# Kernel optimization log

Hardware: AMD Instinct MI355X
Metric: run time of the kernel (lower is better)

The kernel has to match this reference:

```python
import jax, jax.numpy as jnp
import numpy as np

N_CHANNELS = 22
N_PATCHES = 64
N_NODES = N_CHANNELS * N_PATCHES  # 1408
EMBED_DIM = 256
N_HEADS = 4
HEAD_DIM = EMBED_DIM // N_HEADS
ALPHA = 0.15
TOP_P = 0.85
DIST_THRESH = 0.55
BATCH = 16

TCP_PAIRS = [('FP1','F7'),('F7','T3'),('T3','T5'),('T5','O1'),('FP2','F8'),('F8','T4'),('T4','T6'),('T6','O2'),('FP1','F3'),('F3','C3'),('C3','P3'),('P3','O1'),('FP2','F4'),('F4','C4'),('C4','P4'),('P4','O2'),('A1','T3'),('T3','C3'),('C3','CZ'),('CZ','C4'),('C4','T4'),('T4','A2')]
_ELECTRODE_3D = {'FP1':(-0.31,0.95,0.0),'FP2':(0.31,0.95,0.0),'F7':(-0.81,0.59,0.0),'F3':(-0.55,0.67,0.5),'FZ':(0.0,0.71,0.71),'F4':(0.55,0.67,0.5),'F8':(0.81,0.59,0.0),'T3':(-1.0,0.0,0.0),'C3':(-0.57,0.0,0.82),'CZ':(0.0,0.0,1.0),'C4':(0.57,0.0,0.82),'T4':(1.0,0.0,0.0),'T5':(-0.81,-0.59,0.0),'P3':(-0.55,-0.67,0.5),'PZ':(0.0,-0.71,0.71),'P4':(0.55,-0.67,0.5),'T6':(0.81,-0.59,0.0),'O1':(-0.31,-0.95,0.0),'O2':(0.31,-0.95,0.0),'A1':(-1.05,0.0,-0.3),'A2':(1.05,0.0,-0.3)}


def _build_masks():
    # channel positions = midpoint of each bipolar TCP pair -> [22,3]
    ch_pos = np.array([(np.array(_ELECTRODE_3D[a]) + np.array(_ELECTRODE_3D[b])) / 2.0 for a, b in TCP_PAIRS])
    d = np.linalg.norm(ch_pos[:, None, :] - ch_pos[None, :, :], axis=-1)
    ch_adj = (d < DIST_THRESH).astype(np.float32)
    np.fill_diagonal(ch_adj, 0.0)
    # node = ch * n_patches + t ; spatial edges only between same t: kron(ch_adj, I_P)
    spatial = np.kron(ch_adj, np.eye(N_PATCHES, dtype=np.float32))
    # temporal: same channel, |p - p'| == 1
    T = np.zeros((N_PATCHES, N_PATCHES), dtype=np.float32)
    idx = np.arange(N_PATCHES - 1)
    T[idx, idx + 1] = 1.0
    T[idx + 1, idx] = 1.0
    temporal = np.kron(np.eye(N_CHANNELS, dtype=np.float32), T)
    return jnp.asarray(temporal), jnp.asarray(spatial)


def setup_inputs() -> dict:
    key = jax.random.key(0)
    ks = jax.random.split(key, 8)
    D, H, HD = EMBED_DIM, N_HEADS, HEAD_DIM
    s = 1.0 / np.sqrt(D)
    x = jax.random.normal(ks[0], (BATCH, N_NODES, D), dtype=jnp.float32)
    proj_w = jax.random.uniform(ks[1], (H, HD, D), jnp.float32, -s, s)
    gate_w = jax.random.uniform(ks[2], (3, D), jnp.float32, -s, s)
    gate_b = jax.random.uniform(ks[3], (3,), jnp.float32, -s, s)
    score_w1 = jax.random.uniform(ks[4], (D // 2, D), jnp.float32, -s, s)
    score_b1 = jax.random.uniform(ks[5], (D // 2,), jnp.float32, -s, s)
    s2 = 1.0 / np.sqrt(D // 2)
    score_w2 = jax.random.uniform(ks[6], (1, D // 2), jnp.float32, -s2, s2)
    score_b2 = jax.random.uniform(ks[7], (1,), jnp.float32, -s2, s2)
    threshold = jnp.asarray(0.5, dtype=jnp.float32)
    temporal_mask, spatial_mask = _build_masks()
    return {"x": x, "proj_w": proj_w, "gate_w": gate_w, "gate_b": gate_b,
            "score_w1": score_w1, "score_b1": score_b1, "score_w2": score_w2,
            "score_b2": score_b2, "threshold": threshold,
            "temporal_mask": temporal_mask, "spatial_mask": spatial_mask}


def _safe_dist(d2):
    d2 = jnp.maximum(d2, 0.0)
    return jnp.where(d2 > 0, jnp.sqrt(jnp.where(d2 > 0, d2, 1.0)), 0.0)


def reference(x, proj_w, gate_w, gate_b, score_w1, score_b1, score_w2, score_b2,
              threshold, temporal_mask, spatial_mask):
    B, N, D = x.shape
    H = proj_w.shape[0]
    k = max(1, int(N * ALPHA))
    b_idx = jnp.arange(B)[:, None, None]
    r_idx = jnp.arange(N)[None, :, None]

    # ---- MultiHeadDistanceKNN: mean over heads of (knn-mask * gaussian sim) ----
    adj = jnp.zeros((B, N, N), x.dtype)
    for h in range(H):
        z = x @ proj_w[h].T                                  # [B,N,hd]
        sq = jnp.sum(z * z, axis=-1)                         # [B,N]
        d2 = sq[:, :, None] + sq[:, None, :] - 2.0 * jnp.einsum('bnd,bmd->bnm', z, z)
        dist = _safe_dist(d2)                                # [B,N,N]
        _, topk_idx = jax.lax.top_k(-dist, k)                # k smallest dists
        m = jnp.zeros((B, N, N), x.dtype).at[b_idx, r_idx, topk_idx].set(1.0)
        m = jnp.maximum(m, jnp.swapaxes(m, -1, -2))          # symmetrize
        sim = jnp.exp(-dist * dist / (2.0 * jnp.mean(dist) ** 2 + 1e-8))
        adj = adj + sim * m
    adj = adj / H

    # ---- Temporal / Spatial filters (fixed masks) ----
    adj_t = adj * temporal_mask[None]
    adj_s = adj * spatial_mask[None]

    # ---- Pathological filter: MLP node score -> outer product -> soft gate ----
    h1 = jax.nn.gelu(x @ score_w1.T + score_b1, approximate=False)
    scores = jax.nn.sigmoid((h1 @ score_w2.T + score_b2)[..., 0])    # [B,N]
    edge_w = scores[:, :, None] * scores[:, None, :]
    adj_p = adj * jax.nn.sigmoid((edge_w - threshold) * 10.0)

    # ---- NoisyGatedRouter (eval: no noise): softmax -> top-p truncate -> renorm ----
    probs = jax.nn.softmax(x @ gate_w.T + gate_b, axis=-1)           # [B,N,3]
    order = jnp.argsort(-probs, axis=-1)
    sp = jnp.take_along_axis(probs, order, axis=-1)
    keep = (jnp.cumsum(sp, axis=-1) - sp) < TOP_P
    sp = sp * keep.astype(sp.dtype)
    inv = jnp.argsort(order, axis=-1)
    w = jnp.take_along_axis(sp, inv, axis=-1)                        # scatter back
    w = w / (jnp.sum(w, axis=-1, keepdims=True) + 1e-8)              # [B,N,3]

    # ---- Mix filters with per-edge weights (w_i + w_j)/2 ----
    out = jnp.zeros_like(adj)
    for f, a in enumerate((adj_t, adj_s, adj_p)):
        wf = w[:, :, f]
        ewf = (wf[:, :, None] + wf[:, None, :]) * 0.5
        out = out + a * ewf
    return out
```

## Files before the change

### kernel.cpp

```cpp
#include <hip/hip_runtime.h>
#include <math.h>

typedef __attribute__((ext_vector_type(8))) short bf16x8;
typedef __attribute__((ext_vector_type(4))) float f32x4;

__device__ __forceinline__ float wsum64(float v) {
#pragma unroll
  for (int d = 32; d > 0; d >>= 1) v += __shfl_xor(v, d, 64);
  return v;
}

__device__ __forceinline__ unsigned short f2bf(float f) {
  unsigned u = __float_as_uint(f);
  u = (u + 0x7FFFu + ((u >> 16) & 1u)) >> 16;
  return (unsigned short)u;
}

__global__ void k_init(const float* __restrict__ smask, float* __restrict__ chadj,
                       double* __restrict__ sums) {
  int t = threadIdx.x;
  if (t < 4) sums[t] = 0.0;
  if (t < 484) {
    int c1 = t / 22, c2 = t % 22;
    chadj[t] = smask[(size_t)(c1 * 64) * 1408 + (size_t)c2 * 64];
  }
}

__global__ __launch_bounds__(256) void k_gemm_in(
    const float* __restrict__ x, const float* __restrict__ projw,
    const float* __restrict__ w1, float* __restrict__ z, float* __restrict__ zT,
    unsigned short* __restrict__ zb, float* __restrict__ h1) {
  __shared__ float xs[16][68];
  __shared__ float wsT[16][68];
  __shared__ float ldsT[64][65];
  int n0 = blockIdx.x * 64;
  int o0 = blockIdx.y * 64;
  int tid = threadIdx.x;
  int tx = tid & 15, ty = tid >> 4;
  float acc[4][4];
#pragma unroll
  for (int i = 0; i < 4; i++)
#pragma unroll
    for (int j = 0; j < 4; j++) acc[i][j] = 0.f;
  for (int kc = 0; kc < 16; kc++) {
#pragma unroll
    for (int rep = 0; rep < 4; rep++) {
      int e = tid + rep * 256;
      int n = e >> 4, k = e & 15;
      xs[k][n] = x[(size_t)(n0 + n) * 256 + kc * 16 + k];
      int row = o0 + n;
      wsT[k][n] = (row < 256) ? projw[(size_t)row * 256 + kc * 16 + k]
                              : w1[(size_t)(row - 256) * 256 + kc * 16 + k];
    }
    __syncthreads();
#pragma unroll
    for (int k = 0; k < 16; k++) {
      float4 a4 = *(const float4*)&xs[k][4 * ty];
      float4 w4 = *(const float4*)&wsT[k][4 * tx];
      float ar[4] = {a4.x, a4.y, a4.z, a4.w};
      float wr[4] = {w4.x, w4.y, w4.z, w4.w};
#pragma unroll
      for (int i = 0; i < 4; i++)
#pragma unroll
        for (int j = 0; j < 4; j++) acc[i][j] = fmaf(ar[i], wr[j], acc[i][j]);
    }
    __syncthreads();
  }
  if (blockIdx.y >= 4) {
#pragma unroll
    for (int i = 0; i < 4; i++) {
      size_t base = (size_t)(n0 + 4 * ty + i) * 128 + (o0 - 256) + 4 * tx;
      float4 t;
      t.x = acc[i][0]; t.y = acc[i][1]; t.z = acc[i][2]; t.w = acc[i][3];
      *(float4*)&h1[base] = t;
    }
  } else {
#pragma unroll
    for (int i = 0; i < 4; i++) {
      size_t base = (size_t)(n0 + 4 * ty + i) * 256 + o0 + 4 * tx;
      float4 t;
      t.x = acc[i][0]; t.y = acc[i][1]; t.z = acc[i][2]; t.w = acc[i][3];
      *(float4*)&z[base] = t;
      unsigned lo = (unsigned)f2bf(acc[i][0]) | ((unsigned)f2bf(acc[i][1]) << 16);
      unsigned hi = (unsigned)f2bf(acc[i][2]) | ((unsigned)f2bf(acc[i][3]) << 16);
      uint2 u2; u2.x = lo; u2.y = hi;
      *(uint2*)(zb + base) = u2;
    }
    __syncthreads();
#pragma unroll
    for (int i = 0; i < 4; i++)
#pragma unroll
      for (int j = 0; j < 4; j++) ldsT[4 * tx + j][4 * ty + i] = acc[i][j];
    __syncthreads();
    int bblk = blockIdx.x / 22;
    int nbase = (blockIdx.x % 22) * 64;
#pragma unroll
    for (int rep = 0; rep < 16; rep++) {
      int e = tid + rep * 256;
      int oo = e >> 6, nn = e & 63;
      zT[(size_t)((bblk * 4 + blockIdx.y) * 64 + oo) * 1408 + nbase + nn] = ldsT[oo][nn];
    }
  }
}

__global__ __launch_bounds__(256) void k_node(
    const float* __restrict__ x, const float* __restrict__ z,
    const float* __restrict__ h1, const float* __restrict__ gw,
    const float* __restrict__ gb, const float* __restrict__ b1,
    const float* __restrict__ w2, const float* __restrict__ b2v,
    float* __restrict__ sq, float4* __restrict__ wnode) {
  int tid = threadIdx.x;
  int w = tid >> 6, lane = tid & 63;
  int node = blockIdx.x * 4 + w;
  int b = node / 1408, n = node % 1408;
  const float* zr = z + (size_t)node * 256;
  const float* xr = x + (size_t)node * 256;
#pragma unroll
  for (int c = 0; c < 4; c++) {
    float val = zr[c * 64 + lane];
    float s = wsum64(val * val);
    if (lane == 0) sq[(size_t)(b * 4 + c) * 1408 + n] = s;
  }
  float gl[3];
#pragma unroll
  for (int f = 0; f < 3; f++) {
    float p = 0.f;
#pragma unroll
    for (int c = 0; c < 4; c++)
      p = fmaf(xr[c * 64 + lane], gw[f * 256 + c * 64 + lane], p);
    gl[f] = wsum64(p) + gb[f];
  }
  const float* hr = h1 + (size_t)node * 128;
  float ps = 0.f;
#pragma unroll
  for (int c = 0; c < 2; c++) {
    float t = hr[c * 64 + lane] + b1[c * 64 + lane];
    float g = 0.5f * t * (1.f + erff(t * 0.7071067811865475f));
    ps = fmaf(g, w2[c * 64 + lane], ps);
  }
  float sc = wsum64(ps) + b2v[0];
  sc = 1.f / (1.f + expf(-sc));
  float mx = fmaxf(gl[0], fmaxf(gl[1], gl[2]));
  float ex[3];
  float esum = 0.f;
#pragma unroll
  for (int f = 0; f < 3; f++) { ex[f] = expf(gl[f] - mx); esum += ex[f]; }
  float p3[3];
#pragma unroll
  for (int f = 0; f < 3; f++) p3[f] = ex[f] / esum;
  int rk[3];
#pragma unroll
  for (int f = 0; f < 3; f++) {
    int r = 0;
#pragma unroll
    for (int g = 0; g < 3; g++)
      r += ((p3[g] > p3[f]) || (p3[g] == p3[f] && g < f)) ? 1 : 0;
    rk[f] = r;
  }
  float sp[3]; int oi[3];
#pragma unroll
  for (int f = 0; f < 3; f++) { sp[rk[f]] = p3[f]; oi[rk[f]] = f; }
  bool k1 = sp[0] < 0.85f;
  bool k2 = (sp[0] + sp[1]) < 0.85f;
  float wv[3];
  wv[oi[0]] = sp[0];
  wv[oi[1]] = k1 ? sp[1] : 0.f;
  wv[oi[2]] = k2 ? sp[2] : 0.f;
  float inv = 1.f / (wv[0] + wv[1] + wv[2] + 1e-8f);
  if (lane == 0) wnode[node] = make_float4(wv[0] * inv, wv[1] * inv, wv[2] * inv, sc);
}

template <int TC>
__device__ __forceinline__ void dotstrip16(float (&v)[16][6],
                                           const float* __restrict__ zTh,
                                           const float (&As)[64][16], int jb) {
#pragma unroll
  for (int r = 0; r < 16; r++)
#pragma unroll
    for (int t = 0; t < TC; t++) v[r][t] = 0.f;
  const float* bp = zTh + jb;
  float b0[TC], b1[TC];
#pragma unroll
  for (int t = 0; t < TC; t++) b0[t] = bp[t * 64];
#pragma unroll
  for (int t = 0; t < TC; t++) b1[t] = bp[1408 + t * 64];
  const float* pn = bp + 2 * 1408;
#pragma unroll 1
  for (int k = 0; k < 62; k += 2) {
    float n0[TC], n1[TC];
#pragma unroll
    for (int t = 0; t < TC; t++) n0[t] = pn[t * 64];
    {
      float4 a0 = *(const float4*)&As[k][0];
      float4 a1 = *(const float4*)&As[k][4];
      float4 a2 = *(const float4*)&As[k][8];
      float4 a3 = *(const float4*)&As[k][12];
      float ar[16] = {a0.x, a0.y, a0.z, a0.w, a1.x, a1.y, a1.z, a1.w,
                      a2.x, a2.y, a2.z, a2.w, a3.x, a3.y, a3.z, a3.w};
#pragma unroll
      for (int r = 0; r < 16; r++)
#pragma unroll
        for (int t = 0; t < TC; t++) v[r][t] = fmaf(ar[r], b0[t], v[r][t]);
    }
#pragma unroll
    for (int t = 0; t < TC; t++) n1[t] = pn[1408 + t * 64];
    {
      float4 a0 = *(const float4*)&As[k + 1][0];
      float4 a1 = *(const float4*)&As[k + 1][4];
      float4 a2 = *(const float4*)&As[k + 1][8];
      float4 a3 = *(const float4*)&As[k + 1][12];
      float ar[16] = {a0.x, a0.y, a0.z, a0.w, a1.x, a1.y, a1.z, a1.w,
                      a2.x, a2.y, a2.z, a2.w, a3.x, a3.y, a3.z, a3.w};
#pragma unroll
      for (int r = 0; r < 16; r++)
#pragma unroll
        for (int t = 0; t < TC; t++) v[r][t] = fmaf(ar[r], b1[t], v[r][t]);
    }
    pn += 2 * 1408;
#pragma unroll
    for (int t = 0; t < TC; t++) { b0[t] = n0[t]; b1[t] = n1[t]; }
  }
  {
    float4 a0 = *(const float4*)&As[62][0];
    float4 a1 = *(const float4*)&As[62][4];
    float4 a2 = *(const float4*)&As[62][8];
    float4 a3 = *(const float4*)&As[62][12];
    float ar[16] = {a0.x, a0.y, a0.z, a0.w, a1.x, a1.y, a1.z, a1.w,
                    a2.x, a2.y, a2.z, a2.w, a3.x, a3.y, a3.z, a3.w};
#pragma unroll
    for (int r = 0; r < 16; r++)
#pragma unroll
      for (int t = 0; t < TC; t++) v[r][t] = fmaf(ar[r], b0[t], v[r][t]);
  }
  {
    float4 a0 = *(const float4*)&As[63][0];
    float4 a1 = *(const float4*)&As[63][4];
    float4 a2 = *(const float4*)&As[63][8];
    float4 a3 = *(const float4*)&As[63][12];
    float ar[16] = {a0.x, a0.y, a0.z, a0.w, a1.x, a1.y, a1.z, a1.w,
                    a2.x, a2.y, a2.z, a2.w, a3.x, a3.y, a3.z, a3.w};
#pragma unroll
    for (int r = 0; r < 16; r++)
#pragma unroll
      for (int t = 0; t < TC; t++) v[r][t] = fmaf(ar[r], b1[t], v[r][t]);
  }
}

__global__ __launch_bounds__(256, 2) void k_pass1(
    const float* __restrict__ zT, const float* __restrict__ sq,
    unsigned* __restrict__ bm, double* __restrict__ sums) {
  __shared__ float As[64][16];
  __shared__ float srowL[16];
  __shared__ unsigned hist[8][528];
  __shared__ float cand[16][128];
  __shared__ unsigned candCnt[16];
  __shared__ int tbinS[16], rstarS[16];
  __shared__ float TS[16];
  int b = blockIdx.y, h = blockIdx.z;
  int i0 = blockIdx.x * 16;
  int tid = threadIdx.x;
  int w = tid >> 6, lane = tid & 63;
  const float* zTh = zT + (size_t)((b * 4 + h) * 64) * 1408;
  const float* sqh = sq + (size_t)(b * 4 + h) * 1408;
#pragma unroll
  for (int rep = 0; rep < 4; rep++) {
    int e = tid + rep * 256;
    int k = e >> 4, r = e & 15;
    As[k][r] = zTh[(size_t)k * 1408 + i0 + r];
  }
  if (tid < 16) srowL[tid] = sqh[i0 + tid];
  {
    unsigned* histF = &hist[0][0];
    for (int u = tid; u < 8 * 528; u += 256) histF[u] = 0u;
  }
  if (tid < 16) candCnt[tid] = 0u;
  __syncthreads();

  const int TC = (w < 2) ? 6 : 5;
  const int tbase = (w < 2) ? 6 * w : 5 * w + 2;
  int jb = tbase * 64 + lane;
  float sqj[6];
#pragma unroll
  for (int t = 0; t < 6; t++)
    sqj[t] = (t < 5 || TC == 6) ? sqh[jb + t * 64] : 0.f;

  float v[16][6];
  if (w < 2) dotstrip16<6>(v, zTh, As, jb);
  else       dotstrip16<5>(v, zTh, As, jb);

  float ssum = 0.f;
#pragma unroll
  for (int r = 0; r < 16; r++) {
    float sr = srowL[r];
#pragma unroll
    for (int t = 0; t < 6; t++) {
      if (t < 5 || TC == 6) {
        float d = sr + sqj[t] - 2.f * v[r][t];
        d = fmaxf(d, 0.f);
        ssum += sqrtf(d);
        v[r][t] = d;
        unsigned key = (unsigned)fminf(d * 4.0f, 511.0f);
        atomicAdd(&hist[r >> 1][key + (key >> 6)], 1u << ((r & 1) * 16));
      }
    }
  }
  __syncthreads();

#pragma unroll 1
  for (int q = 0; q < 4; q++) {
    int r = 4 * w + q;
    int sh = (r & 1) * 16;
    const unsigned* hrow = hist[r >> 1];
    unsigned partial = 0;
#pragma unroll
    for (int u = 0; u < 8; u++) {
      int bin = 8 * lane + u;
      partial += (hrow[bin + (bin >> 6)] >> sh) & 0xffffu;
    }
    unsigned inc = partial;
#pragma unroll
    for (int d = 1; d < 64; d <<= 1) {
      unsigned u2 = __shfl_up(inc, d, 64);
      if (lane >= d) inc += u2;
    }
    unsigned long long mk = __ballot(inc >= 211u);
    int Ls = __ffsll(mk) - 1;
    unsigned cbefore = (Ls > 0) ? (unsigned)__shfl((int)inc, Ls - 1, 64) : 0u;
    int tb = -1;
    unsigned run = cbefore, cbelow = cbefore;
#pragma unroll
    for (int u = 0; u < 8; u++) {
      int bin = 8 * Ls + u;
      unsigned c = (hrow[bin + (bin >> 6)] >> sh) & 0xffffu;
      if (tb < 0) {
        if (run + c >= 211u) { tb = bin; cbelow = run; }
        run += c;
      }
    }
    if (lane == 0) { tbinS[r] = tb; rstarS[r] = 211 - (int)cbelow; }
  }
  __syncthreads();

#pragma unroll
  for (int r = 0; r < 16; r++) {
    int tb = tbinS[r];
#pragma unroll
    for (int t = 0; t < 6; t++) {
      if (t < 5 || TC == 6) {
        float d = v[r][t];
        unsigned key = (unsigned)fminf(d * 4.0f, 511.0f);
        if ((int)key == tb) {
          unsigned id = atomicAdd(&candCnt[r], 1u);
          if (id < 128u) cand[r][id] = d;
        }
      }
    }
  }
  __syncthreads();

#pragma unroll 1
  for (int q = 0; q < 4; q++) {
    int r = 4 * w + q;
    int rstar = rstarS[r];
    unsigned craw = candCnt[r];
    int cnt = (craw > 128u) ? 128 : (int)craw;
    float t2l = INFINITY;
    for (int base = 0; base < cnt; base += 64) {
      int ci = base + lane;
      if (ci < cnt) {
        float xm = cand[r][ci];
        int below = 0, eq = 0;
        for (int m = 0; m < cnt; m++) {
          float y = cand[r][m];
          below += (y < xm) ? 1 : 0;
          eq += (y == xm) ? 1 : 0;
        }
        if (below < rstar && rstar <= below + eq) t2l = fminf(t2l, xm);
      }
    }
#pragma unroll
    for (int dd = 32; dd > 0; dd >>= 1) t2l = fminf(t2l, __shfl_xor(t2l, dd, 64));
    if (lane == 0) TS[r] = t2l;
  }
  __syncthreads();

#pragma unroll
  for (int r = 0; r < 16; r++) {
    float T = TS[r];
    unsigned* bmrow = bm + (size_t)((h * 16 + b) * 1408 + i0 + r) * 44;
#pragma unroll
    for (int t = 0; t < 6; t++) {
      if (t < 5 || TC == 6) {
        unsigned long long bl = __ballot(v[r][t] <= T);
        int tile = tbase + t;
        if (lane == 0) bmrow[tile * 2] = (unsigned)bl;
        if (lane == 32) bmrow[tile * 2 + 1] = (unsigned)(bl >> 32);
      }
    }
  }
  ssum = wsum64(ssum);
  if (lane == 0) atomicAdd(&sums[h], (double)ssum);
}

__global__ __launch_bounds__(256) void k_final(
    const unsigned short* __restrict__ zb, const float* __restrict__ sq,
    const float4* __restrict__ wnode, const unsigned* __restrict__ bm,
    const double* __restrict__ sums, const float* __restrict__ chadj,
    const float* __restrict__ thrp, float* __restrict__ out) {
  int it = blockIdx.x, jt = blockIdx.y, b = blockIdx.z;
  int tid = threadIdx.x, wv = tid >> 6, lane = tid & 63;
  int quad = lane >> 4, l15 = lane & 15;
  float c2h[4];
#pragma unroll
  for (int h = 0; h < 4; h++) {
    double mu = sums[h] * (1.0 / (16.0 * 1408.0 * 1408.0));
    c2h[h] = (float)(1.0 / (2.0 * mu * mu + 1e-8)) * 1.44269504088896f;
  }
  float thr = thrp[0];
  int ib = it * 64 + wv * 16;
  const unsigned short* za = zb + (size_t)(b * 1408 + ib + l15) * 256;
  bf16x8 af[4][2];
#pragma unroll
  for (int h = 0; h < 4; h++)
#pragma unroll
    for (int k0 = 0; k0 < 2; k0++)
      af[h][k0] = *(const bf16x8*)(za + h * 64 + k0 * 32 + quad * 8);
  int ibq = ib + quad * 4;
  float4 wi[4];
  float sqi[4][4];
#pragma unroll
  for (int reg = 0; reg < 4; reg++) {
    int i = ibq + reg;
    wi[reg] = wnode[b * 1408 + i];
#pragma unroll
    for (int h = 0; h < 4; h++) sqi[reg][h] = sq[(size_t)(b * 4 + h) * 1408 + i];
  }
#pragma unroll
  for (int js = 0; js < 4; js++) {
    int j = jt * 64 + js * 16 + l15;
    const unsigned short* zj = zb + (size_t)(b * 1408 + j) * 256;
    f32x4 acc[4];
#pragma unroll
    for (int h = 0; h < 4; h++) {
      bf16x8 b0 = *(const bf16x8*)(zj + h * 64 + quad * 8);
      bf16x8 b1f = *(const bf16x8*)(zj + h * 64 + 32 + quad * 8);
      f32x4 a = {0.f, 0.f, 0.f, 0.f};
      a = __builtin_amdgcn_mfma_f32_16x16x32_bf16(af[h][0], b0, a, 0, 0, 0);
      a = __builtin_amdgcn_mfma_f32_16x16x32_bf16(af[h][1], b1f, a, 0, 0, 0);
      acc[h] = a;
    }
    float sqj[4];
#pragma unroll
    for (int h = 0; h < 4; h++) sqj[h] = sq[(size_t)(b * 4 + h) * 1408 + j];
    float4 wj = wnode[b * 1408 + j];
    float adjv[4] = {0.f, 0.f, 0.f, 0.f};
#pragma unroll
    for (int h = 0; h < 4; h++) {
      const unsigned* bmh = bm + (size_t)(h * 16 + b) * 1408 * 44;
      unsigned wJ = bmh[(size_t)j * 44 + (ibq >> 5)];
#pragma unroll
      for (int reg = 0; reg < 4; reg++) {
        int i = ibq + reg;
        float d2 = sqi[reg][h] + sqj[h] - 2.f * acc[h][reg];
        d2 = fmaxf(d2, 0.f);
        float sim = exp2f(-d2 * c2h[h]);
        unsigned bi = bmh[(size_t)i * 44 + (j >> 5)] >> (j & 31);
        unsigned bj = wJ >> (i & 31);
        adjv[reg] += (((bi | bj) & 1u) != 0u) ? sim : 0.f;
      }
    }
#pragma unroll
    for (int reg = 0; reg < 4; reg++) {
      int i = ibq + reg;
      int chi = i >> 6, pi = i & 63, chj = j >> 6, pj = j & 63;
      float e0 = 0.5f * (wi[reg].x + wj.x);
      float e1 = 0.5f * (wi[reg].y + wj.y);
      float e2 = 0.5f * (wi[reg].z + wj.z);
      float a2 = 0.f;
      if (chi == chj) {
        int dp = pi - pj;
        if (dp == 1 || dp == -1) a2 += e0;
      }
      if (pi == pj && chadj[chi * 22 + chj] != 0.f) a2 += e1;
      float xw = (wi[reg].w * wj.w - thr) * 10.f;
      float pt = 1.f / (1.f + exp2f(-xw * 1.44269504088896f));
      a2 += pt * e2;
      out[(size_t)(b * 1408 + i) * 1408 + j] = 0.25f * adjv[reg] * a2;
    }
  }
}

extern "C" void kernel_launch(void* const* d_in, const int* in_sizes, int n_in,
                              void* d_out, int out_size, void* d_ws, size_t ws_size,
                              hipStream_t stream) {
  (void)in_sizes; (void)n_in; (void)out_size; (void)ws_size;
  const float* x = (const float*)d_in[0];
  const float* projw = (const float*)d_in[1];
  const float* gw = (const float*)d_in[2];
  const float* gb = (const float*)d_in[3];
  const float* w1 = (const float*)d_in[4];
  const float* b1 = (const float*)d_in[5];
  const float* w2 = (const float*)d_in[6];
  const float* b2 = (const float*)d_in[7];
  const float* thr = (const float*)d_in[8];
  const float* smask = (const float*)d_in[10];
  float* out = (float*)d_out;
  char* ws = (char*)d_ws;
  size_t off = 0;
  auto take = [&](size_t bytes) {
    char* p = ws + off;
    off += (bytes + 255) & ~(size_t)255;
    return p;
  };
  float* z = (float*)take((size_t)22528 * 256 * 4);
  float* zT = (float*)take((size_t)22528 * 256 * 4);
  unsigned short* zb = (unsigned short*)take((size_t)22528 * 256 * 2);
  float* h1 = (float*)take((size_t)22528 * 128 * 4);
  float* sq = (float*)take((size_t)16 * 4 * 1408 * 4);
  float4* wnode = (float4*)take((size_t)22528 * 16);
  unsigned* bm = (unsigned*)take((size_t)4 * 16 * 1408 * 44 * 4);
  float* chadj = (float*)take(484 * 4);
  double* sums = (double*)take(4 * 8);

  hipLaunchKernelGGL(k_init, dim3(1), dim3(512), 0, stream, smask, chadj, sums);
  hipLaunchKernelGGL(k_gemm_in, dim3(352, 6), dim3(256), 0, stream, x, projw, w1,
                     z, zT, zb, h1);
  hipLaunchKernelGGL(k_node, dim3(5632), dim3(256), 0, stream, x, z, h1, gw, gb,
                     b1, w2, b2, sq, wnode);
  hipLaunchKernelGGL(k_pass1, dim3(88, 16, 4), dim3(256), 0, stream, zT, sq, bm,
                     sums);
  hipLaunchKernelGGL(k_final, dim3(22, 22, 16), dim3(256), 0, stream, zb, sq,
                     wnode, bm, sums, chadj, thr, out);
}
```

Before: 997.8 us.

## Split k_pass1 rows across two waves per column strip with 512-thread blocks

k_pass1 now runs 8 waves per block, with each pair of waves sharing a column strip and each wave handling 8 of the 16 rows. This halves the per-thread accumulator array, from 96 to 48 floats, which cuts register pressure and lets the launch bounds ask for 4 blocks of 512 threads. The cost is that each B-column load from global memory is repeated by two waves instead of being reused across all 16 rows, and the block-wide barriers now span more waves.

Measured after the change: 1.075 ms. +7.8%, slower.

```diff
diff --git a/kernel.cpp b/kernel.cpp
--- a/kernel.cpp
+++ b/kernel.cpp
@@ -171,11 +171,12 @@
 }
 
 template <int TC>
-__device__ __forceinline__ void dotstrip16(float (&v)[16][6],
-                                           const float* __restrict__ zTh,
-                                           const float (&As)[64][16], int jb) {
-#pragma unroll
-  for (int r = 0; r < 16; r++)
+__device__ __forceinline__ void dotstrip8(float (&v)[8][6],
+                                          const float* __restrict__ zTh,
+                                          const float (&As)[64][16], int jb,
+                                          int rbase) {
+#pragma unroll
+  for (int r = 0; r < 8; r++)
 #pragma unroll
     for (int t = 0; t < TC; t++) v[r][t] = 0.f;
   const float* bp = zTh + jb;
@@ -191,28 +192,22 @@
 #pragma unroll
     for (int t = 0; t < TC; t++) n0[t] = pn[t * 64];
     {
-      float4 a0 = *(const float4*)&As[k][0];
-      float4 a1 = *(const float4*)&As[k][4];
-      float4 a2 = *(const float4*)&As[k][8];
-      float4 a3 = *(const float4*)&As[k][12];
-      float ar[16] = {a0.x, a0.y, a0.z, a0.w, a1.x, a1.y, a1.z, a1.w,
-                      a2.x, a2.y, a2.z, a2.w, a3.x, a3.y, a3.z, a3.w};
-#pragma unroll
-      for (int r = 0; r < 16; r++)
+      float4 a0 = *(const float4*)&As[k][rbase];
+      float4 a1 = *(const float4*)&As[k][rbase + 4];
+      float ar[8] = {a0.x, a0.y, a0.z, a0.w, a1.x, a1.y, a1.z, a1.w};
+#pragma unroll
+      for (int r = 0; r < 8; r++)
 #pragma unroll
         for (int t = 0; t < TC; t++) v[r][t] = fmaf(ar[r], b0[t], v[r][t]);
     }
 #pragma unroll
     for (int t = 0; t < TC; t++) n1[t] = pn[1408 + t * 64];
     {
-      float4 a0 = *(const float4*)&As[k + 1][0];
-      float4 a1 = *(const float4*)&As[k + 1][4];
-      float4 a2 = *(const float4*)&As[k + 1][8];
-      float4 a3 = *(const float4*)&As[k + 1][12];
-      float ar[16] = {a0.x, a0.y, a0.z, a0.w, a1.x, a1.y, a1.z, a1.w,
-                      a2.x, a2.y, a2.z, a2.w, a3.x, a3.y, a3.z, a3.w};
-#pragma unroll
-      for (int r = 0; r < 16; r++)
+      float4 a0 = *(const float4*)&As[k + 1][rbase];
+      float4 a1 = *(const float4*)&As[k + 1][rbase + 4];
+      float ar[8] = {a0.x, a0.y, a0.z, a0.w, a1.x, a1.y, a1.z, a1.w};
+#pragma unroll
+      for (int r = 0; r < 8; r++)
 #pragma unroll
         for (int t = 0; t < TC; t++) v[r][t] = fmaf(ar[r], b1[t], v[r][t]);
     }
@@ -221,32 +216,26 @@
     for (int t = 0; t < TC; t++) { b0[t] = n0[t]; b1[t] = n1[t]; }
   }
   {
-    float4 a0 = *(const float4*)&As[62][0];
-    float4 a1 = *(const float4*)&As[62][4];
-    float4 a2 = *(const float4*)&As[62][8];
-    float4 a3 = *(const float4*)&As[62][12];
-    float ar[16] = {a0.x, a0.y, a0.z, a0.w, a1.x, a1.y, a1.z, a1.w,
-                    a2.x, a2.y, a2.z, a2.w, a3.x, a3.y, a3.z, a3.w};
-#pragma unroll
-    for (int r = 0; r < 16; r++)
+    float4 a0 = *(const float4*)&As[62][rbase];
+    float4 a1 = *(const float4*)&As[62][rbase + 4];
+    float ar[8] = {a0.x, a0.y, a0.z, a0.w, a1.x, a1.y, a1.z, a1.w};
+#pragma unroll
+    for (int r = 0; r < 8; r++)
 #pragma unroll
       for (int t = 0; t < TC; t++) v[r][t] = fmaf(ar[r], b0[t], v[r][t]);
   }
   {
-    float4 a0 = *(const float4*)&As[63][0];
-    float4 a1 = *(const float4*)&As[63][4];
-    float4 a2 = *(const float4*)&As[63][8];
-    float4 a3 = *(const float4*)&As[63][12];
-    float ar[16] = {a0.x, a0.y, a0.z, a0.w, a1.x, a1.y, a1.z, a1.w,
-                    a2.x, a2.y, a2.z, a2.w, a3.x, a3.y, a3.z, a3.w};
-#pragma unroll
-    for (int r = 0; r < 16; r++)
+    float4 a0 = *(const float4*)&As[63][rbase];
+    float4 a1 = *(const float4*)&As[63][rbase + 4];
+    float ar[8] = {a0.x, a0.y, a0.z, a0.w, a1.x, a1.y, a1.z, a1.w};
+#pragma unroll
+    for (int r = 0; r < 8; r++)
 #pragma unroll
       for (int t = 0; t < TC; t++) v[r][t] = fmaf(ar[r], b1[t], v[r][t]);
   }
 }
 
-__global__ __launch_bounds__(256, 2) void k_pass1(
+__global__ __launch_bounds__(512, 4) void k_pass1(
     const float* __restrict__ zT, const float* __restrict__ sq,
     unsigned* __restrict__ bm, double* __restrict__ sums) {
   __shared__ float As[64][16];
@@ -263,35 +252,38 @@
   const float* zTh = zT + (size_t)((b * 4 + h) * 64) * 1408;
   const float* sqh = sq + (size_t)(b * 4 + h) * 1408;
 #pragma unroll
-  for (int rep = 0; rep < 4; rep++) {
-    int e = tid + rep * 256;
+  for (int rep = 0; rep < 2; rep++) {
+    int e = tid + rep * 512;
     int k = e >> 4, r = e & 15;
     As[k][r] = zTh[(size_t)k * 1408 + i0 + r];
   }
   if (tid < 16) srowL[tid] = sqh[i0 + tid];
   {
     unsigned* histF = &hist[0][0];
-    for (int u = tid; u < 8 * 528; u += 256) histF[u] = 0u;
+    for (int u = tid; u < 8 * 528; u += 512) histF[u] = 0u;
   }
   if (tid < 16) candCnt[tid] = 0u;
   __syncthreads();
 
-  const int TC = (w < 2) ? 6 : 5;
-  const int tbase = (w < 2) ? 6 * w : 5 * w + 2;
+  const int p = w >> 1;
+  const int rbase = (w & 1) * 8;
+  const int TC = (p < 2) ? 6 : 5;
+  const int tbase = (p < 2) ? 6 * p : 5 * p + 2;
   int jb = tbase * 64 + lane;
   float sqj[6];
 #pragma unroll
   for (int t = 0; t < 6; t++)
     sqj[t] = (t < 5 || TC == 6) ? sqh[jb + t * 64] : 0.f;
 
-  float v[16][6];
-  if (w < 2) dotstrip16<6>(v, zTh, As, jb);
-  else       dotstrip16<5>(v, zTh, As, jb);
+  float v[8][6];
+  if (p < 2) dotstrip8<6>(v, zTh, As, jb, rbase);
+  else       dotstrip8<5>(v, zTh, As, jb, rbase);
 
   float ssum = 0.f;
 #pragma unroll
-  for (int r = 0; r < 16; r++) {
-    float sr = srowL[r];
+  for (int r = 0; r < 8; r++) {
+    int row = rbase + r;
+    float sr = srowL[row];
 #pragma unroll
     for (int t = 0; t < 6; t++) {
       if (t < 5 || TC == 6) {
@@ -300,15 +292,15 @@
         ssum += sqrtf(d);
         v[r][t] = d;
         unsigned key = (unsigned)fminf(d * 4.0f, 511.0f);
-        atomicAdd(&hist[r >> 1][key + (key >> 6)], 1u << ((r & 1) * 16));
+        atomicAdd(&hist[row >> 1][key + (key >> 6)], 1u << ((row & 1) * 16));
       }
     }
   }
   __syncthreads();
 
 #pragma unroll 1
-  for (int q = 0; q < 4; q++) {
-    int r = 4 * w + q;
+  for (int q = 0; q < 2; q++) {
+    int r = 2 * w + q;
     int sh = (r & 1) * 16;
     const unsigned* hrow = hist[r >> 1];
     unsigned partial = 0;
@@ -342,16 +334,17 @@
   __syncthreads();
 
 #pragma unroll
-  for (int r = 0; r < 16; r++) {
-    int tb = tbinS[r];
+  for (int r = 0; r < 8; r++) {
+    int row = rbase + r;
+    int tb = tbinS[row];
 #pragma unroll
     for (int t = 0; t < 6; t++) {
       if (t < 5 || TC == 6) {
         float d = v[r][t];
         unsigned key = (unsigned)fminf(d * 4.0f, 511.0f);
         if ((int)key == tb) {
-          unsigned id = atomicAdd(&candCnt[r], 1u);
-          if (id < 128u) cand[r][id] = d;
+          unsigned id = atomicAdd(&candCnt[row], 1u);
+          if (id < 128u) cand[row][id] = d;
         }
       }
     }
@@ -359,8 +352,8 @@
   __syncthreads();
 
 #pragma unroll 1
-  for (int q = 0; q < 4; q++) {
-    int r = 4 * w + q;
+  for (int q = 0; q < 2; q++) {
+    int r = 2 * w + q;
     int rstar = rstarS[r];
     unsigned craw = candCnt[r];
     int cnt = (craw > 128u) ? 128 : (int)craw;
@@ -385,9 +378,10 @@
   __syncthreads();
 
 #pragma unroll
-  for (int r = 0; r < 16; r++) {
-    float T = TS[r];
-    unsigned* bmrow = bm + (size_t)((h * 16 + b) * 1408 + i0 + r) * 44;
+  for (int r = 0; r < 8; r++) {
+    int row = rbase + r;
+    float T = TS[row];
+    unsigned* bmrow = bm + (size_t)((h * 16 + b) * 1408 + i0 + row) * 44;
 #pragma unroll
     for (int t = 0; t < 6; t++) {
       if (t < 5 || TC == 6) {
@@ -527,7 +521,7 @@
                      z, zT, zb, h1);
   hipLaunchKernelGGL(k_node, dim3(5632), dim3(256), 0, stream, x, z, h1, gw, gb,
                      b1, w2, b2, sq, wnode);
-  hipLaunchKernelGGL(k_pass1, dim3(88, 16, 4), dim3(256), 0, stream, zT, sq, bm,
+  hipLaunchKernelGGL(k_pass1, dim3(88, 16, 4), dim3(512), 0, stream, zT, sq, bm,
                      sums);
   hipLaunchKernelGGL(k_final, dim3(22, 22, 16), dim3(256), 0, stream, zb, sq,
                      wnode, bm, sums, chadj, thr, out);
```
